# Optimization experiments

Hardware: AMD Instinct MI355X
Metric: run time of the kernel (lower is better)

Reference implementation:

```python
import jax, jax.numpy as jnp
import numpy as np

N_USERS, N_ITEMS, N_GROUPS = 20000, 20000, 2000
MAX_M, D, K, B = 20, 64, 2, 8192


def setup_inputs() -> dict:
    key = jax.random.key(0)
    ks = jax.random.split(key, 12)
    membership = jax.random.randint(ks[0], (N_GROUPS, MAX_M), 0, N_USERS)
    member_mask = jnp.zeros((N_GROUPS, MAX_M), jnp.float32)  # exp -> all-ones weights
    # binary group-member incidence consistent with membership (dedupes duplicates)
    hyper_graph = jnp.zeros((N_GROUPS, N_USERS), jnp.float32)
    hyper_graph = hyper_graph.at[jnp.arange(N_GROUPS)[:, None], membership].set(1.0)
    user_emb = 0.1 * jax.random.normal(ks[1], (N_USERS, D), jnp.float32)
    item_emb = 0.1 * jax.random.normal(ks[2], (N_ITEMS, D), jnp.float32)
    Wk = 0.05 * jax.random.normal(ks[3], (K, D, 2 * D), jnp.float32)
    bk = jnp.zeros((K, D), jnp.float32)
    p1w = 0.1 * jax.random.normal(ks[4], (16, D), jnp.float32)
    p1b = jnp.zeros((16,), jnp.float32)
    p2w = 0.1 * jax.random.normal(ks[5], (1, 16), jnp.float32)
    p2b = jnp.zeros((1,), jnp.float32)
    groups = jax.random.randint(ks[6], (B,), 0, N_GROUPS)
    items = jax.random.randint(ks[7], (B,), 0, N_ITEMS)
    return dict(groups=groups, items=items, membership=membership,
                member_mask=member_mask, hyper_graph=hyper_graph,
                user_emb=user_emb, item_emb=item_emb, Wk=Wk, bk=bk,
                p1w=p1w, p1b=p1b, p2w=p2w, p2b=p2b)


def _l2norm(x, eps=1e-12):
    return x / jnp.maximum(jnp.linalg.norm(x, axis=-1, keepdims=True), eps)


def reference(groups, items, membership, member_mask, hyper_graph,
              user_emb, item_emb, Wk, bk, p1w, p1b, p2w, p2b):
    # masked-mean group embedding from member users: [G, D]
    w = jnp.exp(member_mask)                                  # [G, M]
    g_users = user_emb[membership]                            # [G, M, D]
    emb = (g_users * w[..., None]).sum(1) / w.sum(1, keepdims=True)
    # group adjacency = common-member counts, zero diagonal
    adj = hyper_graph @ hyper_graph.T                         # [G, G]
    adj = adj - jnp.diag(jnp.diag(adj))
    # Vectorized set-intersection message: for binary H, common count == adj[i,j],
    # so sum_j adj[i,j] * mean(U[common(i,j)]) = sum_j (H_i * H_j) @ U (j != i)
    #                                          = (H * H.sum(0) - H) @ U
    deg = hyper_graph.sum(0)                                  # [n_users]
    neigh_member = (hyper_graph * deg[None, :] - hyper_graph) @ user_emb  # [G, D]
    for i in range(K):
        neigh_group = adj @ emb                               # [G, D]
        msg = neigh_group + neigh_member
        emb = jnp.concatenate([emb, msg], axis=1) @ Wk[i].T + bk[i]
        emb = _l2norm(emb)
    ge = emb[groups]                                          # [B, D]
    ie = item_emb[items]                                      # [B, D]
    h = jax.nn.relu((ge * ie) @ p1w.T + p1b)                  # [B, 16]
    return jax.nn.sigmoid(h @ p2w.T + p2b)                    # [B, 1]
```

## Files before the change

### kernel.cpp

```cpp
#include <hip/hip_runtime.h>
#include <math.h>

#define D 64
#define MAXM 20
#define CAP 32
#define CAPS 64

__global__ void zero_kernel(int* __restrict__ p, int n) {
  const int i = blockIdx.x * blockDim.x + threadIdx.x;
  if (i < n) p[i] = 0;
}

__global__ void init_kernel(const int* __restrict__ membership,
                            const float* __restrict__ member_mask,
                            const float* __restrict__ user_emb,
                            const int* __restrict__ groups,
                            float* __restrict__ emb0,
                            unsigned int* __restrict__ ufm,
                            int* __restrict__ deg, int* __restrict__ inv,
                            int* __restrict__ scnt, int* __restrict__ sidx,
                            int G, int B) {
  const int g = blockIdx.x;
  const int lane = threadIdx.x;
  __shared__ int   mem[MAXM];
  __shared__ float wgt[MAXM];
  if (lane < MAXM) {
    mem[lane] = membership[g * MAXM + lane];
    wgt[lane] = expf(member_mask[g * MAXM + lane]);
  }
  __syncthreads();

  float acc = 0.f, wsum = 0.f;
#pragma unroll
  for (int m = 0; m < MAXM; ++m) {
    acc  += wgt[m] * user_emb[(long)mem[m] * D + lane];
    wsum += wgt[m];
  }
  emb0[(long)g * D + lane] = acc / wsum;

  bool uniq = false;
  if (lane < MAXM) {
    const int u = mem[lane];
    uniq = true;
    for (int m = 0; m < lane; ++m)
      if (mem[m] == u) uniq = false;
  }
  const unsigned long long bal = __ballot(uniq);
  if (lane == 0) ufm[g] = (unsigned int)bal;
  if (uniq) {
    const int u = mem[lane];
    const int pos = atomicAdd(&deg[u], 1);
    if (pos < CAP) inv[(long)u * CAP + pos] = g;
  }

  for (int s = g * 64 + lane; s < B; s += G * 64) {
    const int gg = groups[s];
    const int pos = atomicAdd(&scnt[gg], 1);
    if (pos < CAPS) sidx[gg * CAPS + pos] = s;
  }
}

__device__ __forceinline__ float update_core(
    const int* __restrict__ membership, const unsigned int* __restrict__ ufm,
    const int* __restrict__ deg, const int* __restrict__ inv,
    const float* __restrict__ user_emb, float* __restrict__ nm, int compute_nm,
    const float* __restrict__ Wk, const float* __restrict__ bk, int k,
    const float* __restrict__ cur, int g, int lane,
    int* mem, float* coef, float* e_sh, float* ms_sh, int* nbr) {
  if (lane < MAXM) mem[lane] = membership[g * MAXM + lane];
  __syncthreads();
  const unsigned int um = ufm[g];
  const float ucnt = (float)__popc(um);
  const float ein = cur[(long)g * D + lane];
  e_sh[lane] = ein;

  int d = 0, u = 0;
  if (lane < MAXM && ((um >> lane) & 1u)) { u = mem[lane]; d = deg[u]; }
  if (compute_nm && lane < MAXM)
    coef[lane] = ((um >> lane) & 1u) ? (float)(d - 1) : 0.f;
  const int dc = d < CAP ? d : CAP;
  int incl = dc;
#pragma unroll
  for (int off = 1; off < 64; off <<= 1) {
    const int v = __shfl_up(incl, off);
    if (lane >= off) incl += v;
  }
  const int total = __shfl(incl, 63);
  const int base = incl - dc;
  for (int i = 0; i < dc; ++i) nbr[base + i] = inv[(long)u * CAP + i];
  __syncthreads();

  float ng = 0.f;
  int i = 0;
  for (; i + 4 <= total; i += 4) {
    const int n0 = nbr[i], n1 = nbr[i + 1], n2 = nbr[i + 2], n3 = nbr[i + 3];
    const float a0 = cur[(long)n0 * D + lane];
    const float a1 = cur[(long)n1 * D + lane];
    const float a2 = cur[(long)n2 * D + lane];
    const float a3 = cur[(long)n3 * D + lane];
    ng += (a0 + a1) + (a2 + a3);
  }
  for (; i < total; ++i) ng += cur[(long)nbr[i] * D + lane];

  float nmv;
  if (compute_nm) {
    nmv = 0.f;
#pragma unroll
    for (int m = 0; m < MAXM; ++m)
      nmv += coef[m] * user_emb[(long)mem[m] * D + lane];
    nm[(long)g * D + lane] = nmv;
  } else {
    nmv = nm[(long)g * D + lane];
  }
  ms_sh[lane] = ng - ucnt * ein + nmv;
  __syncthreads();

  const float* Wrow = Wk + ((long)k * D + lane) * (2 * D);
  float o = bk[k * D + lane];
#pragma unroll
  for (int j = 0; j < D; ++j)
    o += e_sh[j] * Wrow[j] + ms_sh[j] * Wrow[D + j];
  float ss = o * o;
#pragma unroll
  for (int sh = 32; sh; sh >>= 1) ss += __shfl_xor(ss, sh);
  return o * (1.f / fmaxf(sqrtf(ss), 1e-12f));
}

__global__ void upd_kernel(const int* __restrict__ membership,
                           const unsigned int* __restrict__ ufm,
                           const int* __restrict__ deg,
                           const int* __restrict__ inv,
                           const float* __restrict__ user_emb,
                           float* __restrict__ nm, int compute_nm,
                           const float* __restrict__ Wk,
                           const float* __restrict__ bk, int k,
                           const float* __restrict__ cur,
                           float* __restrict__ nxt) {
  const int g = blockIdx.x, lane = threadIdx.x;
  __shared__ int   mem[MAXM];
  __shared__ float coef[MAXM];
  __shared__ float e_sh[D], ms_sh[D];
  __shared__ int   nbr[MAXM * CAP];
  const float o = update_core(membership, ufm, deg, inv, user_emb, nm,
                              compute_nm, Wk, bk, k, cur, g, lane,
                              mem, coef, e_sh, ms_sh, nbr);
  nxt[(long)g * D + lane] = o;
}

__global__ void upd_head_kernel(const int* __restrict__ membership,
                                const unsigned int* __restrict__ ufm,
                                const int* __restrict__ deg,
                                const int* __restrict__ inv,
                                const float* __restrict__ user_emb,
                                float* __restrict__ nm, int compute_nm,
                                const float* __restrict__ Wk,
                                const float* __restrict__ bk, int k,
                                const float* __restrict__ cur,
                                const int* __restrict__ scnt,
                                const int* __restrict__ sidx,
                                const int* __restrict__ items,
                                const float* __restrict__ item_emb,
                                const float* __restrict__ p1w,
                                const float* __restrict__ p1b,
                                const float* __restrict__ p2w,
                                const float* __restrict__ p2b,
                                float* __restrict__ out) {
  const int g = blockIdx.x, lane = threadIdx.x;
  __shared__ int   mem[MAXM];
  __shared__ float coef[MAXM];
  __shared__ float e_sh[D], ms_sh[D];
  __shared__ int   nbr[MAXM * CAP];
  const float o = update_core(membership, ufm, deg, inv, user_emb, nm,
                              compute_nm, Wk, bk, k, cur, g, lane,
                              mem, coef, e_sh, ms_sh, nbr);

  const int ns0 = scnt[g];
  const int ns = ns0 < CAPS ? ns0 : CAPS;
  if (ns > 0) {
    float p1r[16], p1br[16], p2wr[16];
#pragma unroll
    for (int j = 0; j < 16; ++j) {
      p1r[j]  = p1w[j * D + lane];
      p1br[j] = p1b[j];
      p2wr[j] = p2w[j];
    }
    const float p2b0 = p2b[0];
    for (int si = 0; si < ns; ++si) {
      const int s  = sidx[g * CAPS + si];
      const int it = items[s];
      const float x = o * item_emb[(long)it * D + lane];
      float pv[16];
#pragma unroll
      for (int j = 0; j < 16; ++j) pv[j] = x * p1r[j];
#pragma unroll
      for (int off = 32; off; off >>= 1) {
#pragma unroll
        for (int j = 0; j < 16; ++j) pv[j] += __shfl_xor(pv[j], off);
      }
      float acc2 = p2b0;
#pragma unroll
      for (int j = 0; j < 16; ++j)
        acc2 += fmaxf(pv[j] + p1br[j], 0.f) * p2wr[j];
      if (lane == 0) out[s] = 1.f / (1.f + expf(-acc2));
    }
  }
}

extern "C" void kernel_launch(void* const* d_in, const int* in_sizes, int n_in,
                              void* d_out, int out_size, void* d_ws, size_t ws_size,
                              hipStream_t stream) {
  const int*   groups      = (const int*)d_in[0];
  const int*   items       = (const int*)d_in[1];
  const int*   membership  = (const int*)d_in[2];
  const float* member_mask = (const float*)d_in[3];
  const float* user_emb    = (const float*)d_in[5];
  const float* item_emb    = (const float*)d_in[6];
  const float* Wk          = (const float*)d_in[7];
  const float* bk          = (const float*)d_in[8];
  const float* p1w         = (const float*)d_in[9];
  const float* p1b         = (const float*)d_in[10];
  const float* p2w         = (const float*)d_in[11];
  const float* p2b         = (const float*)d_in[12];
  float* out = (float*)d_out;

  const int B  = in_sizes[0];
  const int G  = in_sizes[2] / MAXM;
  const int NU = in_sizes[5] / D;
  const int K  = in_sizes[7] / (D * 2 * D);

  char* ws = (char*)d_ws;
  float*        emb_a = (float*)ws;        ws += (size_t)G * D * 4;
  float*        emb_b = (float*)ws;        ws += (size_t)G * D * 4;
  float*        nm    = (float*)ws;        ws += (size_t)G * D * 4;
  int*          deg   = (int*)ws;          ws += (size_t)NU * 4;
  int*          scnt  = (int*)ws;          ws += (size_t)G * 4;
  int*          inv   = (int*)ws;          ws += (size_t)NU * CAP * 4;
  int*          sidx  = (int*)ws;          ws += (size_t)G * CAPS * 4;
  unsigned int* ufm   = (unsigned int*)ws; ws += (size_t)G * 4;

  zero_kernel<<<(NU + G + 255) / 256, 256, 0, stream>>>(deg, NU + G);
  init_kernel<<<G, 64, 0, stream>>>(membership, member_mask, user_emb, groups,
                                    emb_a, ufm, deg, inv, scnt, sidx, G, B);

  float* cur = emb_a;
  float* nxt = emb_b;
  for (int k = 0; k < K - 1; ++k) {
    upd_kernel<<<G, 64, 0, stream>>>(membership, ufm, deg, inv, user_emb,
                                     nm, (k == 0) ? 1 : 0, Wk, bk, k, cur, nxt);
    float* tmp = cur; cur = nxt; nxt = tmp;
  }
  upd_head_kernel<<<G, 64, 0, stream>>>(
      membership, ufm, deg, inv, user_emb, nm, (K == 1) ? 1 : 0, Wk, bk, K - 1,
      cur, scnt, sidx, items, item_emb, p1w, p1b, p2w, p2b, out);
}
```

Before: 60.12 us.

## Pack four groups per block, float4 gathers, and balance head work across warps

Each 256-thread block now handles four groups, one per wavefront, instead of one 64-thread block per group. Row gathers (user embeddings, neighbour rows, Wk) use float4 loads with 16 lanes per row, so four rows are fetched per instruction and then combined with xor shuffles. Neighbour lists are padded to a multiple of four with self-indices, and the extra self terms are subtracted through alpha. The head's scoring samples are pooled across the block's four warps to balance load. The zero kernel becomes a hipMemsetAsync. The cost is more shared memory per block and extra block-wide syncs.

```diff
diff --git a/kernel.cpp b/kernel.cpp
--- a/kernel.cpp
+++ b/kernel.cpp
@@ -5,55 +5,71 @@
 #define MAXM 20
 #define CAP 32
 #define CAPS 64
-
-__global__ void zero_kernel(int* __restrict__ p, int n) {
-  const int i = blockIdx.x * blockDim.x + threadIdx.x;
-  if (i < n) p[i] = 0;
-}
-
-__global__ void init_kernel(const int* __restrict__ membership,
-                            const float* __restrict__ member_mask,
-                            const float* __restrict__ user_emb,
-                            const int* __restrict__ groups,
-                            float* __restrict__ emb0,
-                            unsigned int* __restrict__ ufm,
-                            int* __restrict__ deg, int* __restrict__ inv,
-                            int* __restrict__ scnt, int* __restrict__ sidx,
-                            int G, int B) {
-  const int g = blockIdx.x;
-  const int lane = threadIdx.x;
-  __shared__ int   mem[MAXM];
-  __shared__ float wgt[MAXM];
-  if (lane < MAXM) {
+#define WPB 4
+#define TPB 256
+
+#define XOR_COMBINE4(v)                                        \
+  do {                                                         \
+    v.x += __shfl_xor(v.x, 16); v.x += __shfl_xor(v.x, 32);    \
+    v.y += __shfl_xor(v.y, 16); v.y += __shfl_xor(v.y, 32);    \
+    v.z += __shfl_xor(v.z, 16); v.z += __shfl_xor(v.z, 32);    \
+    v.w += __shfl_xor(v.w, 16); v.w += __shfl_xor(v.w, 32);    \
+  } while (0)
+
+__global__ __launch_bounds__(TPB) void init_kernel(
+    const int* __restrict__ membership, const float* __restrict__ member_mask,
+    const float* __restrict__ user_emb, const int* __restrict__ groups,
+    float* __restrict__ emb0, unsigned int* __restrict__ ufm,
+    int* __restrict__ deg, int* __restrict__ inv,
+    int* __restrict__ scnt, int* __restrict__ sidx, int G, int B) {
+  const int w    = threadIdx.x >> 6;
+  const int lane = threadIdx.x & 63;
+  const int g    = blockIdx.x * WPB + w;
+  const int sub  = lane >> 4, q = lane & 15;
+  __shared__ int   mem_s[WPB][MAXM];
+  __shared__ float wgt_s[WPB][MAXM];
+  int*   mem = mem_s[w];
+  float* wgt = wgt_s[w];
+  if (g < G && lane < MAXM) {
     mem[lane] = membership[g * MAXM + lane];
     wgt[lane] = expf(member_mask[g * MAXM + lane]);
   }
   __syncthreads();
-
-  float acc = 0.f, wsum = 0.f;
-#pragma unroll
-  for (int m = 0; m < MAXM; ++m) {
-    acc  += wgt[m] * user_emb[(long)mem[m] * D + lane];
-    wsum += wgt[m];
-  }
-  emb0[(long)g * D + lane] = acc / wsum;
-
-  bool uniq = false;
-  if (lane < MAXM) {
-    const int u = mem[lane];
-    uniq = true;
-    for (int m = 0; m < lane; ++m)
-      if (mem[m] == u) uniq = false;
-  }
-  const unsigned long long bal = __ballot(uniq);
-  if (lane == 0) ufm[g] = (unsigned int)bal;
-  if (uniq) {
-    const int u = mem[lane];
-    const int pos = atomicAdd(&deg[u], 1);
-    if (pos < CAP) inv[(long)u * CAP + pos] = g;
-  }
-
-  for (int s = g * 64 + lane; s < B; s += G * 64) {
+  if (g < G) {
+    float wsum = 0.f;
+#pragma unroll
+    for (int m = 0; m < MAXM; ++m) wsum += wgt[m];
+    float4 acc = make_float4(0.f, 0.f, 0.f, 0.f);
+#pragma unroll
+    for (int it = 0; it < MAXM / 4; ++it) {
+      const int m = it * 4 + sub;
+      const float c = wgt[m];
+      const float4 v = *(const float4*)(user_emb + (long)mem[m] * D + q * 4);
+      acc.x += c * v.x; acc.y += c * v.y; acc.z += c * v.z; acc.w += c * v.w;
+    }
+    XOR_COMBINE4(acc);
+    if (lane < 16) {
+      const float iw = 1.f / wsum;
+      float4 r = make_float4(acc.x * iw, acc.y * iw, acc.z * iw, acc.w * iw);
+      ((float4*)(emb0 + (long)g * D))[q] = r;
+    }
+    bool uniq = false;
+    if (lane < MAXM) {
+      const int u = mem[lane];
+      uniq = true;
+      for (int m = 0; m < lane; ++m)
+        if (mem[m] == u) uniq = false;
+    }
+    const unsigned long long bal = __ballot(uniq);
+    if (lane == 0) ufm[g] = (unsigned int)bal;
+    if (uniq) {
+      const int u = mem[lane];
+      const int pos = atomicAdd(&deg[u], 1);
+      if (pos < CAP) inv[(long)u * CAP + pos] = g;
+    }
+  }
+  const int nthreads = gridDim.x * TPB;
+  for (int s = blockIdx.x * TPB + threadIdx.x; s < B; s += nthreads) {
     const int gg = groups[s];
     const int pos = atomicAdd(&scnt[gg], 1);
     if (pos < CAPS) sidx[gg * CAPS + pos] = s;
@@ -67,17 +83,16 @@
     const float* __restrict__ Wk, const float* __restrict__ bk, int k,
     const float* __restrict__ cur, int g, int lane,
     int* mem, float* coef, float* e_sh, float* ms_sh, int* nbr) {
+  const int sub = lane >> 4, q = lane & 15;
   if (lane < MAXM) mem[lane] = membership[g * MAXM + lane];
-  __syncthreads();
   const unsigned int um = ufm[g];
-  const float ucnt = (float)__popc(um);
   const float ein = cur[(long)g * D + lane];
   e_sh[lane] = ein;
 
   int d = 0, u = 0;
-  if (lane < MAXM && ((um >> lane) & 1u)) { u = mem[lane]; d = deg[u]; }
-  if (compute_nm && lane < MAXM)
-    coef[lane] = ((um >> lane) & 1u) ? (float)(d - 1) : 0.f;
+  const bool uq = (lane < MAXM) && ((um >> lane) & 1u);
+  if (uq) { u = mem[lane]; d = deg[u]; }
+  if (lane < MAXM) coef[lane] = uq ? (float)(d - 1) : 0.f;
   const int dc = d < CAP ? d : CAP;
   int incl = dc;
 #pragma unroll
@@ -88,121 +103,152 @@
   const int total = __shfl(incl, 63);
   const int base = incl - dc;
   for (int i = 0; i < dc; ++i) nbr[base + i] = inv[(long)u * CAP + i];
-  __syncthreads();
-
-  float ng = 0.f;
-  int i = 0;
-  for (; i + 4 <= total; i += 4) {
-    const int n0 = nbr[i], n1 = nbr[i + 1], n2 = nbr[i + 2], n3 = nbr[i + 3];
-    const float a0 = cur[(long)n0 * D + lane];
-    const float a1 = cur[(long)n1 * D + lane];
-    const float a2 = cur[(long)n2 * D + lane];
-    const float a3 = cur[(long)n3 * D + lane];
-    ng += (a0 + a1) + (a2 + a3);
-  }
-  for (; i < total; ++i) ng += cur[(long)nbr[i] * D + lane];
-
-  float nmv;
+  const int padc = (4 - (total & 3)) & 3;
+  if (lane < padc) nbr[total + lane] = g;
+  __syncthreads();
+
+  const int T4 = total + padc;
+  float4 ng4 = make_float4(0.f, 0.f, 0.f, 0.f);
+  for (int i = 0; i < T4; i += 4) {
+    const int row = nbr[i + sub];
+    const float4 v = *(const float4*)(cur + (long)row * D + q * 4);
+    ng4.x += v.x; ng4.y += v.y; ng4.z += v.z; ng4.w += v.w;
+  }
+  XOR_COMBINE4(ng4);
+
+  float4 nm4 = make_float4(0.f, 0.f, 0.f, 0.f);
   if (compute_nm) {
-    nmv = 0.f;
-#pragma unroll
-    for (int m = 0; m < MAXM; ++m)
-      nmv += coef[m] * user_emb[(long)mem[m] * D + lane];
-    nm[(long)g * D + lane] = nmv;
-  } else {
-    nmv = nm[(long)g * D + lane];
-  }
-  ms_sh[lane] = ng - ucnt * ein + nmv;
-  __syncthreads();
-
-  const float* Wrow = Wk + ((long)k * D + lane) * (2 * D);
+#pragma unroll
+    for (int it = 0; it < MAXM / 4; ++it) {
+      const int m = it * 4 + sub;
+      const float c = coef[m];
+      const float4 v = *(const float4*)(user_emb + (long)mem[m] * D + q * 4);
+      nm4.x += c * v.x; nm4.y += c * v.y; nm4.z += c * v.z; nm4.w += c * v.w;
+    }
+    XOR_COMBINE4(nm4);
+    if (lane < 16) ((float4*)(nm + (long)g * D))[q] = nm4;
+  }
+  if (lane < 16) {
+    const float4 nmv4 =
+        compute_nm ? nm4 : ((const float4*)(nm + (long)g * D))[q];
+    const float alpha = (float)__popc(um) + (float)padc;
+    const float4 e4 = ((const float4*)e_sh)[q];
+    float4 ms4;
+    ms4.x = ng4.x + nmv4.x - alpha * e4.x;
+    ms4.y = ng4.y + nmv4.y - alpha * e4.y;
+    ms4.z = ng4.z + nmv4.z - alpha * e4.z;
+    ms4.w = ng4.w + nmv4.w - alpha * e4.w;
+    ((float4*)ms_sh)[q] = ms4;
+  }
+  __syncthreads();
+
+  const float4* W4 = (const float4*)(Wk + ((long)k * D + lane) * (2 * D));
+  const float4* e4p = (const float4*)e_sh;
+  const float4* m4p = (const float4*)ms_sh;
   float o = bk[k * D + lane];
 #pragma unroll
-  for (int j = 0; j < D; ++j)
-    o += e_sh[j] * Wrow[j] + ms_sh[j] * Wrow[D + j];
+  for (int j = 0; j < 16; ++j) {
+    const float4 a = e4p[j], wv = W4[j];
+    o += a.x * wv.x + a.y * wv.y + a.z * wv.z + a.w * wv.w;
+  }
+#pragma unroll
+  for (int j = 0; j < 16; ++j) {
+    const float4 a = m4p[j], wv = W4[16 + j];
+    o += a.x * wv.x + a.y * wv.y + a.z * wv.z + a.w * wv.w;
+  }
   float ss = o * o;
 #pragma unroll
   for (int sh = 32; sh; sh >>= 1) ss += __shfl_xor(ss, sh);
   return o * (1.f / fmaxf(sqrtf(ss), 1e-12f));
 }
 
-__global__ void upd_kernel(const int* __restrict__ membership,
-                           const unsigned int* __restrict__ ufm,
-                           const int* __restrict__ deg,
-                           const int* __restrict__ inv,
-                           const float* __restrict__ user_emb,
-                           float* __restrict__ nm, int compute_nm,
-                           const float* __restrict__ Wk,
-                           const float* __restrict__ bk, int k,
-                           const float* __restrict__ cur,
-                           float* __restrict__ nxt) {
-  const int g = blockIdx.x, lane = threadIdx.x;
-  __shared__ int   mem[MAXM];
-  __shared__ float coef[MAXM];
-  __shared__ float e_sh[D], ms_sh[D];
-  __shared__ int   nbr[MAXM * CAP];
+__global__ __launch_bounds__(TPB) void upd_kernel(
+    const int* __restrict__ membership, const unsigned int* __restrict__ ufm,
+    const int* __restrict__ deg, const int* __restrict__ inv,
+    const float* __restrict__ user_emb, float* __restrict__ nm, int compute_nm,
+    const float* __restrict__ Wk, const float* __restrict__ bk, int k,
+    const float* __restrict__ cur, float* __restrict__ nxt, int G) {
+  const int w = threadIdx.x >> 6, lane = threadIdx.x & 63;
+  const int g0 = blockIdx.x * WPB + w;
+  const int g = g0 < G ? g0 : G - 1;
+  __shared__ int   mem_s[WPB][MAXM];
+  __shared__ float coef_s[WPB][MAXM];
+  __shared__ float e_s[WPB][D], ms_s[WPB][D];
+  __shared__ int   nbr_s[WPB][MAXM * CAP + 4];
   const float o = update_core(membership, ufm, deg, inv, user_emb, nm,
                               compute_nm, Wk, bk, k, cur, g, lane,
-                              mem, coef, e_sh, ms_sh, nbr);
-  nxt[(long)g * D + lane] = o;
-}
-
-__global__ void upd_head_kernel(const int* __restrict__ membership,
-                                const unsigned int* __restrict__ ufm,
-                                const int* __restrict__ deg,
-                                const int* __restrict__ inv,
-                                const float* __restrict__ user_emb,
-                                float* __restrict__ nm, int compute_nm,
-                                const float* __restrict__ Wk,
-                                const float* __restrict__ bk, int k,
-                                const float* __restrict__ cur,
-                                const int* __restrict__ scnt,
-                                const int* __restrict__ sidx,
-                                const int* __restrict__ items,
-                                const float* __restrict__ item_emb,
-                                const float* __restrict__ p1w,
-                                const float* __restrict__ p1b,
-                                const float* __restrict__ p2w,
-                                const float* __restrict__ p2b,
-                                float* __restrict__ out) {
-  const int g = blockIdx.x, lane = threadIdx.x;
-  __shared__ int   mem[MAXM];
-  __shared__ float coef[MAXM];
-  __shared__ float e_sh[D], ms_sh[D];
-  __shared__ int   nbr[MAXM * CAP];
+                              mem_s[w], coef_s[w], e_s[w], ms_s[w], nbr_s[w]);
+  if (g0 < G) nxt[(long)g0 * D + lane] = o;
+}
+
+__global__ __launch_bounds__(TPB) void upd_head_kernel(
+    const int* __restrict__ membership, const unsigned int* __restrict__ ufm,
+    const int* __restrict__ deg, const int* __restrict__ inv,
+    const float* __restrict__ user_emb, float* __restrict__ nm, int compute_nm,
+    const float* __restrict__ Wk, const float* __restrict__ bk, int k,
+    const float* __restrict__ cur,
+    const int* __restrict__ scnt, const int* __restrict__ sidx,
+    const int* __restrict__ items, const float* __restrict__ item_emb,
+    const float* __restrict__ p1w, const float* __restrict__ p1b,
+    const float* __restrict__ p2w, const float* __restrict__ p2b,
+    float* __restrict__ out, int G) {
+  const int w = threadIdx.x >> 6, lane = threadIdx.x & 63;
+  const int g0 = blockIdx.x * WPB + w;
+  const int g = g0 < G ? g0 : G - 1;
+  __shared__ int   mem_s[WPB][MAXM];
+  __shared__ float coef_s[WPB][MAXM];
+  __shared__ float e_s[WPB][D], ms_s[WPB][D];
+  __shared__ int   nbr_s[WPB][MAXM * CAP + 4];
   const float o = update_core(membership, ufm, deg, inv, user_emb, nm,
                               compute_nm, Wk, bk, k, cur, g, lane,
-                              mem, coef, e_sh, ms_sh, nbr);
-
-  const int ns0 = scnt[g];
-  const int ns = ns0 < CAPS ? ns0 : CAPS;
-  if (ns > 0) {
-    float p1r[16], p1br[16], p2wr[16];
-#pragma unroll
-    for (int j = 0; j < 16; ++j) {
-      p1r[j]  = p1w[j * D + lane];
-      p1br[j] = p1b[j];
-      p2wr[j] = p2w[j];
-    }
-    const float p2b0 = p2b[0];
-    for (int si = 0; si < ns; ++si) {
-      const int s  = sidx[g * CAPS + si];
-      const int it = items[s];
-      const float x = o * item_emb[(long)it * D + lane];
-      float pv[16];
-#pragma unroll
-      for (int j = 0; j < 16; ++j) pv[j] = x * p1r[j];
-#pragma unroll
-      for (int off = 32; off; off >>= 1) {
-#pragma unroll
-        for (int j = 0; j < 16; ++j) pv[j] += __shfl_xor(pv[j], off);
-      }
-      float acc2 = p2b0;
-#pragma unroll
-      for (int j = 0; j < 16; ++j)
-        acc2 += fmaxf(pv[j] + p1br[j], 0.f) * p2wr[j];
-      if (lane == 0) out[s] = 1.f / (1.f + expf(-acc2));
-    }
+                              mem_s[w], coef_s[w], e_s[w], ms_s[w], nbr_s[w]);
+
+  __shared__ float o_sh[WPB][D];
+  __shared__ int   slist[WPB * CAPS];
+  __shared__ unsigned char sgw[WPB * CAPS];
+  __shared__ int   soff[WPB + 1];
+  __shared__ int   scnt_sh[WPB];
+  o_sh[w][lane] = o;
+  if (lane == 0) scnt_sh[w] = (g0 < G) ? min(scnt[g0], CAPS) : 0;
+  __syncthreads();
+  if (threadIdx.x == 0) {
+    soff[0] = 0;
+    for (int i = 0; i < WPB; ++i) soff[i + 1] = soff[i] + scnt_sh[i];
+  }
+  __syncthreads();
+  const int my = scnt_sh[w];
+  for (int i = lane; i < my; i += 64) {
+    slist[soff[w] + i] = sidx[g0 * CAPS + i];
+    sgw[soff[w] + i] = (unsigned char)w;
+  }
+  __syncthreads();
+  const int T = soff[WPB];
+  if (T == 0) return;
+  float p1r[16], p1br[16], p2wr[16];
+#pragma unroll
+  for (int j = 0; j < 16; ++j) {
+    p1r[j]  = p1w[j * D + lane];
+    p1br[j] = p1b[j];
+    p2wr[j] = p2w[j];
+  }
+  const float p2b0 = p2b[0];
+  for (int e = w; e < T; e += WPB) {
+    const int s = slist[e];
+    const int gw2 = sgw[e];
+    const float x = o_sh[gw2][lane] * item_emb[(long)items[s] * D + lane];
+    float pv[16];
+#pragma unroll
+    for (int j = 0; j < 16; ++j) pv[j] = x * p1r[j];
+#pragma unroll
+    for (int off = 32; off; off >>= 1) {
+#pragma unroll
+      for (int j = 0; j < 16; ++j) pv[j] += __shfl_xor(pv[j], off);
+    }
+    float acc2 = p2b0;
+#pragma unroll
+    for (int j = 0; j < 16; ++j)
+      acc2 += fmaxf(pv[j] + p1br[j], 0.f) * p2wr[j];
+    if (lane == 0) out[s] = 1.f / (1.f + expf(-acc2));
   }
 }
 
@@ -238,18 +284,22 @@
   int*          sidx  = (int*)ws;          ws += (size_t)G * CAPS * 4;
   unsigned int* ufm   = (unsigned int*)ws; ws += (size_t)G * 4;
 
-  zero_kernel<<<(NU + G + 255) / 256, 256, 0, stream>>>(deg, NU + G);
-  init_kernel<<<G, 64, 0, stream>>>(membership, member_mask, user_emb, groups,
-                                    emb_a, ufm, deg, inv, scnt, sidx, G, B);
+  const int nblk = (G + WPB - 1) / WPB;
+
+  hipMemsetAsync(deg, 0, (size_t)(NU + G) * 4, stream);
+  init_kernel<<<nblk, TPB, 0, stream>>>(membership, member_mask, user_emb,
+                                        groups, emb_a, ufm, deg, inv,
+                                        scnt, sidx, G, B);
 
   float* cur = emb_a;
   float* nxt = emb_b;
   for (int k = 0; k < K - 1; ++k) {
-    upd_kernel<<<G, 64, 0, stream>>>(membership, ufm, deg, inv, user_emb,
-                                     nm, (k == 0) ? 1 : 0, Wk, bk, k, cur, nxt);
+    upd_kernel<<<nblk, TPB, 0, stream>>>(membership, ufm, deg, inv, user_emb,
+                                         nm, (k == 0) ? 1 : 0, Wk, bk, k,
+                                         cur, nxt, G);
     float* tmp = cur; cur = nxt; nxt = tmp;
   }
-  upd_head_kernel<<<G, 64, 0, stream>>>(
+  upd_head_kernel<<<nblk, TPB, 0, stream>>>(
       membership, ufm, deg, inv, user_emb, nm, (K == 1) ? 1 : 0, Wk, bk, K - 1,
-      cur, scnt, sidx, items, item_emb, p1w, p1b, p2w, p2b, out);
-}
+      cur, scnt, sidx, items, item_emb, p1w, p1b, p2w, p2b, out, G);
+}
```

Result: faster. 58.57 us (-2.6%).
